# Kernel tuning notes

Measured on AMD Instinct MI355X. Metric: run time of the kernel, lower is better.

The kernel has to match this reference:

```python
import jax, jax.numpy as jnp
import numpy as np

N, E, F_IN, H, G, C = 50000, 800000, 128, 128, 64, 10
EPS = 1e-5


def _glorot_lin(key, fin, fout):
    s = 1.0 / np.sqrt(fin)
    return jax.random.uniform(key, (fin, fout), jnp.float32, -s, s)


def setup_inputs() -> dict:
    key = jax.random.key(0)
    ks = jax.random.split(key, 24)
    x = jax.random.normal(ks[0], (N, F_IN), jnp.float32)
    edge_index = jax.random.randint(ks[1], (2, E), 0, N)
    batch = jnp.sort(jax.random.randint(ks[2], (N,), 0, G))
    inp = {"x": x, "edge_index": edge_index, "batch": batch}
    # GCNConv weights [in, out] and biases
    dims = [(F_IN, H), (H, H), (H, H), (H, H)]
    for i, (fi, fo) in enumerate(dims, start=1):
        inp[f"W{i}"] = _glorot_lin(ks[2 + i], fi, fo)
        inp[f"b{i}"] = jnp.zeros((fo,), jnp.float32)
    # BatchNorm affine params
    for i in range(1, 4):
        inp[f"g{i}"] = jnp.ones((H,), jnp.float32)
        inp[f"be{i}"] = jnp.zeros((H,), jnp.float32)
    # MLP head
    inp["lw1"] = _glorot_lin(ks[10], 2 * H, H)
    inp["lb1"] = jnp.zeros((H,), jnp.float32)
    inp["lw2"] = _glorot_lin(ks[11], H, C)
    inp["lb2"] = jnp.zeros((C,), jnp.float32)
    return inp


def _gcn_conv(h_in, W, b, src, dst, norm_e, self_norm):
    # linear transform then symmetric-normalized aggregation (incl. self loops)
    h = h_in @ W                                            # [N, out]
    agg = jax.ops.segment_sum(h[src] * norm_e[:, None], dst, num_segments=N)
    return agg + h * self_norm[:, None] + b


def _batch_norm(x, gamma, beta):
    mu = jnp.mean(x, axis=0)
    var = jnp.var(x, axis=0)
    return (x - mu) * jax.lax.rsqrt(var + EPS) * gamma + beta


def reference(x, edge_index, batch, W1, b1, W2, b2, W3, b3, W4, b4,
              g1, be1, g2, be2, g3, be3, lw1, lb1, lw2, lb2):
    src, dst = edge_index[0], edge_index[1]
    # degrees with self loops; GCN symmetric normalization
    deg = jax.ops.segment_sum(jnp.ones((E,), jnp.float32), dst, num_segments=N) + 1.0
    dinv = jax.lax.rsqrt(deg)
    norm_e = dinv[src] * dinv[dst]   # per-edge norm
    self_norm = 1.0 / deg            # self-loop norm = dinv*dinv

    h = jax.nn.relu(_batch_norm(_gcn_conv(x, W1, b1, src, dst, norm_e, self_norm), g1, be1))
    h = jax.nn.relu(_batch_norm(_gcn_conv(h, W2, b2, src, dst, norm_e, self_norm), g2, be2))
    h = jax.nn.relu(_batch_norm(_gcn_conv(h, W3, b3, src, dst, norm_e, self_norm), g3, be3))
    h = jax.nn.relu(_gcn_conv(h, W4, b4, src, dst, norm_e, self_norm))

    counts = jax.ops.segment_sum(jnp.ones((N,), jnp.float32), batch, num_segments=G)
    x_mean = jax.ops.segment_sum(h, batch, num_segments=G) / counts[:, None]
    x_max = jax.ops.segment_max(h, batch, num_segments=G)
    z = jnp.concatenate([x_mean, x_max], axis=1)            # [G, 2H]

    z = jax.nn.relu(z @ lw1 + lb1)
    # dropout is identity in eval mode
    return z @ lw2 + lb2                                    # [G, C]
```

## Files before the change

kernel.cpp:

```cpp
#include <hip/hip_runtime.h>

#define N_NODES 50000
#define N_EDGES 800000
#define HID     128
#define NGRAPH  64
#define BN_EPS  1e-5f

__global__ __launch_bounds__(256) void deg_counti_kernel(const int* __restrict__ ei,
                                                         int* __restrict__ degi) {
    int i = blockIdx.x * 256 + threadIdx.x;
    if (i < N_EDGES) atomicAdd(&degi[ei[N_EDGES + i]], 1);
}

__global__ __launch_bounds__(256) void deg_fin_kernel(const int* __restrict__ degi,
                                                      float* __restrict__ dinv) {
    int i = blockIdx.x * 256 + threadIdx.x;
    if (i < N_NODES) dinv[i] = rsqrtf((float)degi[i] + 1.0f);
}

__global__ __launch_bounds__(512) void scan_kernel(const int* __restrict__ degi,
                                                   int* __restrict__ row_start) {
    __shared__ int part[512];
    const int t = threadIdx.x;
    const int per = (N_NODES + 511) / 512;
    const int b0 = t * per;
    int s = 0;
    for (int i = b0; i < b0 + per && i < N_NODES; ++i) s += degi[i];
    part[t] = s;
    __syncthreads();
    if (t == 0) {
        int run = 0;
        for (int i = 0; i < 512; ++i) { int v = part[i]; part[i] = run; run += v; }
    }
    __syncthreads();
    int run = part[t];
    for (int i = b0; i < b0 + per && i < N_NODES; ++i) { row_start[i] = run; run += degi[i]; }
    if (t == 511) row_start[N_NODES] = run;
}

__global__ __launch_bounds__(256) void scatter_kernel(const int* __restrict__ ei,
                                                      const float* __restrict__ dinv,
                                                      const int* __restrict__ row_start,
                                                      int* __restrict__ cursor,
                                                      float2* __restrict__ csr_sw) {
    int e = blockIdx.x * 256 + threadIdx.x;
    if (e >= N_EDGES) return;
    const int src = ei[e];
    const int dst = ei[N_EDGES + e];
    const int pos = row_start[dst] + atomicAdd(&cursor[dst], 1);
    float2 sw;
    sw.x = __int_as_float(src);
    sw.y = dinv[src] * dinv[dst];
    csr_sw[pos] = sw;
}

__global__ __launch_bounds__(256) void bounds_kernel(const int* __restrict__ batch,
                                                     int* __restrict__ bound) {
    int i = blockIdx.x * 256 + threadIdx.x;
    if (i >= N_NODES) return;
    const int b = batch[i];
    if (i == 0) {
        for (int g = 0; g <= b; ++g) bound[g] = 0;
    } else {
        const int pb = batch[i - 1];
        for (int g = pb + 1; g <= b; ++g) bound[g] = i;
    }
    if (i == N_NODES - 1) {
        for (int g = b + 1; g <= NGRAPH; ++g) bound[g] = N_NODES;
    }
}

__global__ __launch_bounds__(256) void gemm_kernel(const float* __restrict__ X,
                                                   const float* __restrict__ W,
                                                   const float* __restrict__ stats,
                                                   const int use_bn,
                                                   float* __restrict__ hout) {
    __shared__ float xs[64][128];
    __shared__ float wsm[32][128];
    const int tid = threadIdx.x;
    const int block_row = blockIdx.x * 64;

    {
        const float4* Xv = (const float4*)(X + (size_t)block_row * HID);
        float4* xsv = (float4*)&xs[0][0];
        int rows_valid = N_NODES - block_row;
        if (rows_valid > 64) rows_valid = 64;
        const int max4 = rows_valid * 32;
        for (int i = tid; i < 64 * 32; i += 256) {
            float4 v = (i < max4) ? Xv[i] : make_float4(0.f, 0.f, 0.f, 0.f);
            if (use_bn) {
                const int c4 = (i & 31) * 4;
                const float4 sc = *(const float4*)(stats + c4);
                const float4 sh = *(const float4*)(stats + HID + c4);
                v.x = fmaxf(fmaf(v.x, sc.x, sh.x), 0.f);
                v.y = fmaxf(fmaf(v.y, sc.y, sh.y), 0.f);
                v.z = fmaxf(fmaf(v.z, sc.z, sh.z), 0.f);
                v.w = fmaxf(fmaf(v.w, sc.w, sh.w), 0.f);
            }
            xsv[i] = v;
        }
    }

    const int cg = (tid & 31) * 4;
    const int r0 = (tid >> 5) * 8;

    float acc[8][4];
#pragma unroll
    for (int r = 0; r < 8; ++r)
#pragma unroll
        for (int j = 0; j < 4; ++j) acc[r][j] = 0.f;

    for (int kc = 0; kc < 4; ++kc) {
        __syncthreads();
        {
            const float4* Wv = (const float4*)(W + kc * 32 * HID);
            float4* wsv = (float4*)&wsm[0][0];
            for (int i = tid; i < 32 * 32; i += 256) wsv[i] = Wv[i];
        }
        __syncthreads();
#pragma unroll
        for (int kk = 0; kk < 32; ++kk) {
            const float4 w4 = *(const float4*)(&wsm[kk][cg]);
            const int k = kc * 32 + kk;
#pragma unroll
            for (int r = 0; r < 8; ++r) {
                const float xv = xs[r0 + r][k];
                acc[r][0] = fmaf(xv, w4.x, acc[r][0]);
                acc[r][1] = fmaf(xv, w4.y, acc[r][1]);
                acc[r][2] = fmaf(xv, w4.z, acc[r][2]);
                acc[r][3] = fmaf(xv, w4.w, acc[r][3]);
            }
        }
    }

#pragma unroll
    for (int r = 0; r < 8; ++r) {
        const int row = block_row + r0 + r;
        if (row < N_NODES)
            *(float4*)(hout + (size_t)row * HID + cg) =
                make_float4(acc[r][0], acc[r][1], acc[r][2], acc[r][3]);
    }
}

__global__ __launch_bounds__(256) void agg_csr_kernel(const int* __restrict__ row_start,
                                                      const float2* __restrict__ csr_sw,
                                                      const float* __restrict__ h,
                                                      const float* __restrict__ dinv,
                                                      const float* __restrict__ bias,
                                                      float* __restrict__ agg) {
    const int node = blockIdx.x * 4 + (threadIdx.x >> 6);
    if (node >= N_NODES) return;
    const int lane = threadIdx.x & 63;
    const int c = lane * 2;
    const int beg = row_start[node];
    const int end = row_start[node + 1];

    const float dv = dinv[node];
    const float sn = dv * dv;
    const float2 hv = *(const float2*)(h + (size_t)node * HID + c);
    const float2 bv = *(const float2*)(bias + c);
    float2 a0 = make_float2(fmaf(hv.x, sn, bv.x), fmaf(hv.y, sn, bv.y));
    float2 a1 = make_float2(0.f, 0.f);
    float2 a2 = make_float2(0.f, 0.f);
    float2 a3 = make_float2(0.f, 0.f);

    int p = beg;
    for (; p + 4 <= end; p += 4) {
        const float2 e0 = csr_sw[p];
        const float2 e1 = csr_sw[p + 1];
        const float2 e2 = csr_sw[p + 2];
        const float2 e3 = csr_sw[p + 3];
        const float2 v0 = *(const float2*)(h + (size_t)__float_as_int(e0.x) * HID + c);
        const float2 v1 = *(const float2*)(h + (size_t)__float_as_int(e1.x) * HID + c);
        const float2 v2 = *(const float2*)(h + (size_t)__float_as_int(e2.x) * HID + c);
        const float2 v3 = *(const float2*)(h + (size_t)__float_as_int(e3.x) * HID + c);
        a0.x = fmaf(v0.x, e0.y, a0.x); a0.y = fmaf(v0.y, e0.y, a0.y);
        a1.x = fmaf(v1.x, e1.y, a1.x); a1.y = fmaf(v1.y, e1.y, a1.y);
        a2.x = fmaf(v2.x, e2.y, a2.x); a2.y = fmaf(v2.y, e2.y, a2.y);
        a3.x = fmaf(v3.x, e3.y, a3.x); a3.y = fmaf(v3.y, e3.y, a3.y);
    }
    for (; p < end; ++p) {
        const float2 e0 = csr_sw[p];
        const float2 v0 = *(const float2*)(h + (size_t)__float_as_int(e0.x) * HID + c);
        a0.x = fmaf(v0.x, e0.y, a0.x); a0.y = fmaf(v0.y, e0.y, a0.y);
    }
    a0.x += (a1.x + a2.x) + a3.x;
    a0.y += (a1.y + a2.y) + a3.y;
    *(float2*)(agg + (size_t)node * HID + c) = a0;
}

__global__ __launch_bounds__(256) void bn_stats_kernel(const float* __restrict__ a,
                                                       float* __restrict__ stats) {
    const int c = threadIdx.x & 127;
    const int half = threadIdx.x >> 7;
    const int row0 = blockIdx.x * 128;
    int rend = row0 + 128;
    if (rend > N_NODES) rend = N_NODES;
    float s = 0.f, sq = 0.f;
    for (int r = row0 + half; r < rend; r += 2) {
        const float v = a[(size_t)r * HID + c];
        s += v;
        sq = fmaf(v, v, sq);
    }
    __shared__ float sh[2][2][128];
    sh[0][half][c] = s;
    sh[1][half][c] = sq;
    __syncthreads();
    if (half == 0) {
        atomicAdd(&stats[c], sh[0][0][c] + sh[0][1][c]);
        atomicAdd(&stats[HID + c], sh[1][0][c] + sh[1][1][c]);
    }
}

__global__ __launch_bounds__(128) void bn_fin_kernel(float* __restrict__ stats,
                                                     const float* __restrict__ gamma,
                                                     const float* __restrict__ beta) {
    const int c = threadIdx.x;
    const float invN = 1.0f / (float)N_NODES;
    const float mu = stats[c] * invN;
    const float var = stats[HID + c] * invN - mu * mu;
    const float scale = rsqrtf(var + BN_EPS) * gamma[c];
    stats[c] = scale;
    stats[HID + c] = fmaf(-mu, scale, beta[c]);
}

__global__ __launch_bounds__(256) void pool_seg_kernel(const float* __restrict__ a,
                                                       const int* __restrict__ bound,
                                                       float* __restrict__ z) {
    const int g = blockIdx.x;
    const int cl = threadIdx.x & 31;
    const int c = blockIdx.y * 32 + cl;
    const int par = threadIdx.x >> 5;
    const int beg = bound[g], end = bound[g + 1];
    float s = 0.f, m = 0.f;
    for (int r = beg + par; r < end; r += 8) {
        const float v = fmaxf(a[(size_t)r * HID + c], 0.f);
        s += v;
        m = fmaxf(m, v);
    }
    __shared__ float ssum[8][32];
    __shared__ float smax[8][32];
    ssum[par][cl] = s;
    smax[par][cl] = m;
    __syncthreads();
    if (par == 0) {
        float ts = 0.f, tm = 0.f;
#pragma unroll
        for (int p = 0; p < 8; ++p) { ts += ssum[p][cl]; tm = fmaxf(tm, smax[p][cl]); }
        const float cntf = (float)(end - beg);
        z[g * 256 + c] = ts / fmaxf(cntf, 1.f);
        z[g * 256 + 128 + c] = tm;
    }
}

__global__ __launch_bounds__(128) void head_kernel(const float* __restrict__ z,
                                                   const float* __restrict__ lw1,
                                                   const float* __restrict__ lb1,
                                                   const float* __restrict__ lw2,
                                                   const float* __restrict__ lb2,
                                                   float* __restrict__ out) {
    __shared__ float zin[256];
    __shared__ float z1[128];
    const int g = blockIdx.x;
    const int t = threadIdx.x;
    zin[t] = z[g * 256 + t];
    zin[128 + t] = z[g * 256 + 128 + t];
    __syncthreads();
    float accv = lb1[t];
#pragma unroll 4
    for (int k = 0; k < 256; ++k) accv = fmaf(zin[k], lw1[k * 128 + t], accv);
    z1[t] = fmaxf(accv, 0.f);
    __syncthreads();
    if (t < 10) {
        float o = lb2[t];
#pragma unroll 4
        for (int k = 0; k < 128; ++k) o = fmaf(z1[k], lw2[k * 10 + t], o);
        out[g * 10 + t] = o;
    }
}

extern "C" void kernel_launch(void* const* d_in, const int* in_sizes, int n_in,
                              void* d_out, int out_size, void* d_ws, size_t ws_size,
                              hipStream_t stream) {
    const float* x     = (const float*)d_in[0];
    const int*   ei    = (const int*)d_in[1];
    const int*   batch = (const int*)d_in[2];
    const float* W[4]  = {(const float*)d_in[3], (const float*)d_in[5],
                          (const float*)d_in[7], (const float*)d_in[9]};
    const float* B[4]  = {(const float*)d_in[4], (const float*)d_in[6],
                          (const float*)d_in[8], (const float*)d_in[10]};
    const float* Gm[3] = {(const float*)d_in[11], (const float*)d_in[13],
                          (const float*)d_in[15]};
    const float* Be[3] = {(const float*)d_in[12], (const float*)d_in[14],
                          (const float*)d_in[16]};
    const float* lw1 = (const float*)d_in[17];
    const float* lb1 = (const float*)d_in[18];
    const float* lw2 = (const float*)d_in[19];
    const float* lb2 = (const float*)d_in[20];

    char* ws = (char*)d_ws;
    float*  dinv      = (float*)ws;
    float*  stats     = (float*)(ws + 50000u * 4);
    float*  z         = (float*)(ws + 50256u * 4);
    int*    degi      = (int*)  (ws + 66640u * 4);
    int*    cursor    = (int*)  (ws + 116640u * 4);
    int*    row_start = (int*)  (ws + 166640u * 4);
    int*    bound     = (int*)  (ws + 216644u * 4);
    float2* csr_sw    = (float2*)(ws + 216712u * 4);
    float*  hbuf      = (float*)(ws + 1816712u * 4);
    float*  abuf      = (float*)(ws + 8216712u * 4);

    hipMemsetAsync(degi, 0, 100000u * sizeof(int), stream);
    deg_counti_kernel<<<(N_EDGES + 255) / 256, 256, 0, stream>>>(ei, degi);
    deg_fin_kernel<<<(N_NODES + 255) / 256, 256, 0, stream>>>(degi, dinv);
    scan_kernel<<<1, 512, 0, stream>>>(degi, row_start);
    scatter_kernel<<<(N_EDGES + 255) / 256, 256, 0, stream>>>(ei, dinv, row_start,
                                                              cursor, csr_sw);
    bounds_kernel<<<(N_NODES + 255) / 256, 256, 0, stream>>>(batch, bound);

    const float* cur = x;
    for (int l = 0; l < 4; ++l) {
        gemm_kernel<<<(N_NODES + 63) / 64, 256, 0, stream>>>(cur, W[l], stats,
                                                             l > 0 ? 1 : 0, hbuf);
        agg_csr_kernel<<<(N_NODES + 3) / 4, 256, 0, stream>>>(row_start, csr_sw, hbuf,
                                                              dinv, B[l], abuf);
        if (l < 3) {
            hipMemsetAsync(stats, 0, 256 * sizeof(float), stream);
            bn_stats_kernel<<<(N_NODES + 127) / 128, 256, 0, stream>>>(abuf, stats);
            bn_fin_kernel<<<1, 128, 0, stream>>>(stats, Gm[l], Be[l]);
        }
        cur = abuf;
    }

    pool_seg_kernel<<<dim3(NGRAPH, 4), 256, 0, stream>>>(abuf, bound, z);
    head_kernel<<<NGRAPH, 128, 0, stream>>>(z, lw1, lb1, lw2, lb2, (float*)d_out);
}
```

Baseline: 827.8 us.

## Replace single-block degree scan with three-phase multi-block parallel scan

The exclusive prefix sum over node degrees ran in one 512-thread block, with each thread walking about 98 consecutive entries serially and thread 0 scanning 512 partials. It becomes a block-level Hillis-Steele scan across 98 blocks, a small scan of the block totals, and an add-back pass. This targets a serialized single-CU step in CSR construction, at the cost of two extra kernel launches and a new workspace region for the partials.

```diff
diff --git a/kernel.cpp b/kernel.cpp
--- a/kernel.cpp
+++ b/kernel.cpp
@@ -5,6 +5,7 @@
 #define HID     128
 #define NGRAPH  64
 #define BN_EPS  1e-5f
+#define SCAN_B  98
 
 __global__ __launch_bounds__(256) void deg_counti_kernel(const int* __restrict__ ei,
                                                          int* __restrict__ degi) {
@@ -18,24 +19,46 @@
     if (i < N_NODES) dinv[i] = rsqrtf((float)degi[i] + 1.0f);
 }
 
-__global__ __launch_bounds__(512) void scan_kernel(const int* __restrict__ degi,
-                                                   int* __restrict__ row_start) {
-    __shared__ int part[512];
+__global__ __launch_bounds__(512) void scan1_kernel(const int* __restrict__ degi,
+                                                    int* __restrict__ row_start,
+                                                    int* __restrict__ partials) {
+    __shared__ int sh[512];
     const int t = threadIdx.x;
-    const int per = (N_NODES + 511) / 512;
-    const int b0 = t * per;
-    int s = 0;
-    for (int i = b0; i < b0 + per && i < N_NODES; ++i) s += degi[i];
-    part[t] = s;
+    const int i = blockIdx.x * 512 + t;
+    const int v = (i < N_NODES) ? degi[i] : 0;
+    sh[t] = v;
+    __syncthreads();
+#pragma unroll
+    for (int off = 1; off < 512; off <<= 1) {
+        const int add = (t >= off) ? sh[t - off] : 0;
+        __syncthreads();
+        sh[t] += add;
+        __syncthreads();
+    }
+    if (i < N_NODES) row_start[i] = sh[t] - v;
+    if (t == 511) partials[blockIdx.x] = sh[511];
+}
+
+__global__ __launch_bounds__(128) void scan2_kernel(int* __restrict__ partials,
+                                                    int* __restrict__ row_start) {
+    __shared__ int sh[SCAN_B + 1];
+    const int t = threadIdx.x;
+    if (t < SCAN_B) sh[t] = partials[t];
     __syncthreads();
     if (t == 0) {
         int run = 0;
-        for (int i = 0; i < 512; ++i) { int v = part[i]; part[i] = run; run += v; }
-    }
-    __syncthreads();
-    int run = part[t];
-    for (int i = b0; i < b0 + per && i < N_NODES; ++i) { row_start[i] = run; run += degi[i]; }
-    if (t == 511) row_start[N_NODES] = run;
+        for (int b = 0; b < SCAN_B; ++b) { const int v = sh[b]; sh[b] = run; run += v; }
+        sh[SCAN_B] = run;
+    }
+    __syncthreads();
+    if (t < SCAN_B) partials[t] = sh[t];
+    if (t == 0) row_start[N_NODES] = sh[SCAN_B];
+}
+
+__global__ __launch_bounds__(512) void scan3_kernel(int* __restrict__ row_start,
+                                                    const int* __restrict__ partials) {
+    const int i = blockIdx.x * 512 + threadIdx.x;
+    if (i < N_NODES) row_start[i] += partials[blockIdx.x];
 }
 
 __global__ __launch_bounds__(256) void scatter_kernel(const int* __restrict__ ei,
@@ -309,11 +332,14 @@
     float2* csr_sw    = (float2*)(ws + 216712u * 4);
     float*  hbuf      = (float*)(ws + 1816712u * 4);
     float*  abuf      = (float*)(ws + 8216712u * 4);
+    int*    partials  = (int*)  (ws + 14616712u * 4);
 
     hipMemsetAsync(degi, 0, 100000u * sizeof(int), stream);
     deg_counti_kernel<<<(N_EDGES + 255) / 256, 256, 0, stream>>>(ei, degi);
     deg_fin_kernel<<<(N_NODES + 255) / 256, 256, 0, stream>>>(degi, dinv);
-    scan_kernel<<<1, 512, 0, stream>>>(degi, row_start);
+    scan1_kernel<<<SCAN_B, 512, 0, stream>>>(degi, row_start, partials);
+    scan2_kernel<<<1, 128, 0, stream>>>(partials, row_start);
+    scan3_kernel<<<SCAN_B, 512, 0, stream>>>(row_start, partials);
     scatter_kernel<<<(N_EDGES + 255) / 256, 256, 0, stream>>>(ei, dinv, row_start,
                                                               cursor, csr_sw);
     bounds_kernel<<<(N_NODES + 255) / 256, 256, 0, stream>>>(batch, bound);
```

Result: faster. 751.0 us (-9.3%).
